# Optimization experiments

Hardware: AMD Instinct MI355X
Metric: run time of the kernel (lower is better)

## Reference

```python
import jax, jax.numpy as jnp
import numpy as np

T, F, H = 2048, 256, 384  # seq_len, input_size, hidden_size


def setup_inputs() -> dict:
    key = jax.random.key(0)
    ks = jax.random.split(key, 16)
    s = 1.0 / np.sqrt(F)
    d = {"x": jax.random.normal(ks[0], (T, F), jnp.float32)}
    names = ["q", "k", "v", "i", "f", "o"]
    for j, n in enumerate(names):
        d[f"W{n}"] = jax.random.uniform(ks[1 + j], (H, F), jnp.float32, -s, s)
        d[f"b{n}"] = jax.random.uniform(ks[7 + j], (H,), jnp.float32, -s, s)
    d["conv_w"] = jax.random.uniform(ks[13], (1, 1, 4), jnp.float32, -0.5, 0.5)
    d["conv_b"] = jax.random.uniform(ks[14], (1,), jnp.float32, -0.5, 0.5)
    return d


def _forward(x, Wq, bq, Wk, bk, Wv, bv, Wi, bi, Wf, bf, Wo, bo, conv_w, conv_b):
    # Conv1d(1->1, kernel=4, padding=(3,3)) along time, per input feature.
    xt = x.T[:, None, :]  # (F, 1, T)  feature axis acts as batch
    y = jax.lax.conv_general_dilated(xt, conv_w, (1,), [(3, 3)])  # (F, 1, T+3)
    xp = (y[:, 0, :] + conv_b[0]).T  # (T+3, F)

    inv_sqrt_h = 1.0 / jnp.sqrt(jnp.asarray(H, xp.dtype))
    # Precompute all per-step projections with dense GEMMs (time-parallel part).
    q = xp @ Wq.T + bq                      # (T+3, H)
    k = (xp @ Wk.T + bk) * inv_sqrt_h       # (T+3, H); extra bias_k is zero-init
    v = xp @ Wv.T + bv
    i = jnp.exp(xp @ Wi.T + bi)
    f = jax.nn.sigmoid(xp @ Wf.T + bf)
    o = jax.nn.sigmoid(xp @ Wo.T + bo)

    def step(carry, inp):
        C, n = carry                         # C: (H,H), n: (H,)
        qt, kt, vt, it, ft, ot = inp
        C = ft * C + it * jnp.outer(vt, kt)  # broadcast over last axis, as original
        n = ft * n + it * kt
        den = jnp.maximum(jnp.abs(jnp.dot(n, qt)), 1.0)
        h = ot * (C @ qt) / den
        return (C, n), h

    init = (jnp.zeros((H, H), xp.dtype), jnp.zeros((H,), xp.dtype))
    _, hs = jax.lax.scan(step, init, (q, k, v, i, f, o))
    return hs[-1]  # return_all=False -> last hidden state, shape (H,)


def reference(x, Wq, bq, Wk, bk, Wv, bv, Wi, bi, Wf, bf, Wo, bo, conv_w, conv_b):
    return _forward(x, Wq, bq, Wk, bk, Wv, bv, Wi, bi, Wf, bf, Wo, bo, conv_w, conv_b)
```

## Files before the change

kernel.cpp:

```cpp
#include <hip/hip_runtime.h>
#include <math.h>

#define T_IN 2048
#define TP   2051
#define F    256
#define H    384
#define BK   16
#define NT2  129
#define NCS  258
#define NC3  257

__device__ __forceinline__ float logsig(float z) {
    return (z >= 0.0f) ? -log1pf(__expf(-z)) : z - log1pf(__expf(z));
}

__global__ __launch_bounds__(256) void k1_conv(const float* __restrict__ x,
                        const float* __restrict__ cw,
                        const float* __restrict__ cb, float* __restrict__ xp) {
    int t = blockIdx.x * 4 + (threadIdx.x >> 6);
    int f4 = threadIdx.x & 63;
    if (t >= TP) return;
    float w[4] = {cw[0], cw[1], cw[2], cw[3]};
    float b = cb[0];
    float4 acc = {b, b, b, b};
    int i0 = t - 3;
    const float4* x4 = (const float4*)x;
    #pragma unroll
    for (int j = 0; j < 4; ++j) {
        int tt = i0 + j;
        if (tt >= 0 && tt < T_IN) {
            float4 xv = x4[tt * 64 + f4];
            acc.x = fmaf(w[j], xv.x, acc.x);
            acc.y = fmaf(w[j], xv.y, acc.y);
            acc.z = fmaf(w[j], xv.z, acc.z);
            acc.w = fmaf(w[j], xv.w, acc.w);
        }
    }
    ((float4*)xp)[t * 64 + f4] = acc;
}

__global__ __launch_bounds__(64) void k2_proj(
    const float* __restrict__ xp,
    const float* __restrict__ Wk, const float* __restrict__ bk,
    const float* __restrict__ Wi, const float* __restrict__ bi,
    const float* __restrict__ Wf, const float* __restrict__ bf,
    float* __restrict__ zk, float* __restrict__ ai, float* __restrict__ lf,
    float* __restrict__ cs) {
    __shared__ float alds[BK][20];
    __shared__ float wlds[3][BK][68];
    __shared__ float csred[4][68];
    int tid = threadIdx.x;
    int t0 = blockIdx.x * 16, b0 = blockIdx.y * 64;
    int tx = tid & 15, ty = tid >> 4;
    const float* Wg[3] = {Wk, Wi, Wf};
    float acc[3][16];
    #pragma unroll
    for (int j = 0; j < 3; ++j)
        #pragma unroll
        for (int u = 0; u < 16; ++u) acc[j][u] = 0.0f;

    int at = tid >> 2;
    int ak = (tid & 3) * 4;

    for (int k0 = 0; k0 < 256; k0 += BK) {
        __syncthreads();
        float4 xv = {0.f, 0.f, 0.f, 0.f};
        if (t0 + at < TP) xv = *(const float4*)&xp[(t0 + at) * 256 + k0 + ak];
        alds[ak + 0][at] = xv.x; alds[ak + 1][at] = xv.y;
        alds[ak + 2][at] = xv.z; alds[ak + 3][at] = xv.w;
        #pragma unroll
        for (int j = 0; j < 3; ++j) {
            #pragma unroll
            for (int h = 0; h < 4; ++h) {
                int row = h * 16 + at;
                float4 wv = *(const float4*)&Wg[j][(b0 + row) * 256 + k0 + ak];
                wlds[j][ak + 0][row] = wv.x; wlds[j][ak + 1][row] = wv.y;
                wlds[j][ak + 2][row] = wv.z; wlds[j][ak + 3][row] = wv.w;
            }
        }
        __syncthreads();
        #pragma unroll
        for (int kk = 0; kk < BK; ++kk) {
            float4 a4 = *(const float4*)&alds[kk][ty * 4];
            #pragma unroll
            for (int j = 0; j < 3; ++j) {
                float4 b4 = *(const float4*)&wlds[j][kk][tx * 4];
                acc[j][0]  = fmaf(a4.x, b4.x, acc[j][0]);
                acc[j][1]  = fmaf(a4.x, b4.y, acc[j][1]);
                acc[j][2]  = fmaf(a4.x, b4.z, acc[j][2]);
                acc[j][3]  = fmaf(a4.x, b4.w, acc[j][3]);
                acc[j][4]  = fmaf(a4.y, b4.x, acc[j][4]);
                acc[j][5]  = fmaf(a4.y, b4.y, acc[j][5]);
                acc[j][6]  = fmaf(a4.y, b4.z, acc[j][6]);
                acc[j][7]  = fmaf(a4.y, b4.w, acc[j][7]);
                acc[j][8]  = fmaf(a4.z, b4.x, acc[j][8]);
                acc[j][9]  = fmaf(a4.z, b4.y, acc[j][9]);
                acc[j][10] = fmaf(a4.z, b4.z, acc[j][10]);
                acc[j][11] = fmaf(a4.z, b4.w, acc[j][11]);
                acc[j][12] = fmaf(a4.w, b4.x, acc[j][12]);
                acc[j][13] = fmaf(a4.w, b4.y, acc[j][13]);
                acc[j][14] = fmaf(a4.w, b4.z, acc[j][14]);
                acc[j][15] = fmaf(a4.w, b4.w, acc[j][15]);
            }
        }
    }
    int bA = b0 + tx * 4;
    float4 bk4 = *(const float4*)&bk[bA];
    float4 bi4 = *(const float4*)&bi[bA];
    float4 bf4 = *(const float4*)&bf[bA];
    const float sc = 0.05103103630798287f;
    float4 lfs = {0.f, 0.f, 0.f, 0.f};
    #pragma unroll
    for (int tt = 0; tt < 4; ++tt) {
        int t = t0 + ty * 4 + tt;
        if (t < TP) {
            int row = t * H + bA;
            int o = tt * 4;
            float4 v;
            v.x = (acc[0][o+0] + bk4.x) * sc; v.y = (acc[0][o+1] + bk4.y) * sc;
            v.z = (acc[0][o+2] + bk4.z) * sc; v.w = (acc[0][o+3] + bk4.w) * sc;
            *(float4*)&zk[row] = v;
            v.x = acc[1][o+0] + bi4.x; v.y = acc[1][o+1] + bi4.y;
            v.z = acc[1][o+2] + bi4.z; v.w = acc[1][o+3] + bi4.w;
            *(float4*)&ai[row] = v;
            float4 l;
            l.x = logsig(acc[2][o+0] + bf4.x); l.y = logsig(acc[2][o+1] + bf4.y);
            l.z = logsig(acc[2][o+2] + bf4.z); l.w = logsig(acc[2][o+3] + bf4.w);
            *(float4*)&lf[row] = l;
            lfs.x += l.x; lfs.y += l.y; lfs.z += l.z; lfs.w += l.w;
        }
    }
    *(float4*)&csred[ty][tx * 4] = lfs;
    __syncthreads();
    {
        float s0 = csred[0][tid] + csred[1][tid];
        float s1 = csred[2][tid] + csred[3][tid];
        cs[(2 * blockIdx.x + 0) * H + b0 + tid] = s0;
        cs[(2 * blockIdx.x + 1) * H + b0 + tid] = s1;
    }
}

__global__ __launch_bounds__(256) void k2b_qo(const float* __restrict__ xp,
        const float* __restrict__ Wq, const float* __restrict__ bq,
        const float* __restrict__ Wo, const float* __restrict__ bo,
        float* __restrict__ q, float* __restrict__ o) {
    int tid = threadIdx.x;
    int lane = tid & 63;
    int row = blockIdx.x * 4 + (tid >> 6);
    float4 xv = *(const float4*)&xp[(TP - 1) * 256 + lane * 4];
    float4 q4 = *(const float4*)&Wq[row * 256 + lane * 4];
    float4 o4 = *(const float4*)&Wo[row * 256 + lane * 4];
    float aq = fmaf(xv.x, q4.x, fmaf(xv.y, q4.y, fmaf(xv.z, q4.z, xv.w * q4.w)));
    float ao = fmaf(xv.x, o4.x, fmaf(xv.y, o4.y, fmaf(xv.z, o4.z, xv.w * o4.w)));
    #pragma unroll
    for (int off = 32; off; off >>= 1) {
        aq += __shfl_down(aq, off, 64);
        ao += __shfl_down(ao, off, 64);
    }
    if (lane == 0) {
        q[row] = aq + bq[row];
        o[row] = 1.0f / (1.0f + __expf(-(ao + bo[row])));
    }
}

__global__ __launch_bounds__(64) void k3b_scan(const float* __restrict__ cs,
                                               float* __restrict__ co) {
    int b = blockIdx.x * 64 + threadIdx.x;
    float L = 0.0f;
    #pragma unroll 16
    for (int c = NCS - 1; c >= 0; --c) {
        co[c * H + b] = L;
        L += cs[c * H + b];
    }
}

__global__ __launch_bounds__(384) void k3_fused(
    const float* __restrict__ ai, const float* __restrict__ lf,
    const float* __restrict__ zk, const float* __restrict__ co,
    const float* __restrict__ q, const float* __restrict__ xp,
    float* __restrict__ zf, float* __restrict__ Gf) {
    __shared__ float zred[6][256];
    __shared__ float gred[6];
    int tid = threadIdx.x;
    int w = tid >> 6, lane = tid & 63;
    int c = blockIdx.x, ts = c * 8;
    float co0 = co[c * H + tid];
    float qb = q[tid];
    float aiv[8], lfv[8], zkv[8];
    float4 xv[8];
    if (ts + 8 <= TP) {
        #pragma unroll
        for (int u = 0; u < 8; ++u) {
            int idx = (ts + u) * H + tid;
            aiv[u] = ai[idx]; lfv[u] = lf[idx]; zkv[u] = zk[idx];
            xv[u] = *(const float4*)&xp[(ts + u) * 256 + lane * 4];
        }
    } else {
        #pragma unroll
        for (int u = 0; u < 8; ++u) {
            if (ts + u < TP) {
                int idx = (ts + u) * H + tid;
                aiv[u] = ai[idx]; lfv[u] = lf[idx]; zkv[u] = zk[idx];
                xv[u] = *(const float4*)&xp[(ts + u) * 256 + lane * 4];
            } else {
                aiv[u] = -1e30f; lfv[u] = 0.f; zkv[u] = 0.f;
                xv[u].x = xv[u].y = xv[u].z = xv[u].w = 0.f;
            }
        }
    }
    float S = 0.f, gsum = 0.f;
    float z0 = 0.f, z1 = 0.f, z2 = 0.f, z3 = 0.f;
    #pragma unroll
    for (int u = 7; u >= 0; --u) {
        float wv = __expf(aiv[u] + co0 + S) * zkv[u] * qb;
        S += lfv[u];
        float s = wv;
        s += __shfl_xor(s, 1, 64);
        s += __shfl_xor(s, 2, 64);
        s += __shfl_xor(s, 4, 64);
        s += __shfl_xor(s, 8, 64);
        s += __shfl_xor(s, 16, 64);
        s += __shfl_xor(s, 32, 64);
        gsum += s;
        z0 = fmaf(s, xv[u].x, z0);
        z1 = fmaf(s, xv[u].y, z1);
        z2 = fmaf(s, xv[u].z, z2);
        z3 = fmaf(s, xv[u].w, z3);
    }
    zred[w][lane * 4 + 0] = z0;
    zred[w][lane * 4 + 1] = z1;
    zred[w][lane * 4 + 2] = z2;
    zred[w][lane * 4 + 3] = z3;
    if (lane == 0) gred[w] = gsum;
    __syncthreads();
    if (tid < 256) {
        float s = zred[0][tid] + zred[1][tid] + zred[2][tid]
                + zred[3][tid] + zred[4][tid] + zred[5][tid];
        atomicAdd(&zf[tid], s);
    }
    if (tid == 0)
        atomicAdd(Gf, gred[0] + gred[1] + gred[2] + gred[3] + gred[4] + gred[5]);
}

__global__ __launch_bounds__(256) void k6_out(const float* __restrict__ zf,
        const float* __restrict__ Gf,
        const float* __restrict__ Wv, const float* __restrict__ bv,
        const float* __restrict__ o, float* __restrict__ out) {
    int tid = threadIdx.x;
    int lane = tid & 63;
    int row = blockIdx.x * 4 + (tid >> 6);
    float Gv = Gf[0];
    float4 zv = *(const float4*)&zf[lane * 4];
    float4 wv = *(const float4*)&Wv[row * 256 + lane * 4];
    float acc = fmaf(zv.x, wv.x, fmaf(zv.y, wv.y, fmaf(zv.z, wv.z, zv.w * wv.w)));
    #pragma unroll
    for (int off = 32; off; off >>= 1) acc += __shfl_down(acc, off, 64);
    if (lane == 0)
        out[row] = o[row] * (acc + bv[row] * Gv) / fmaxf(fabsf(Gv), 1.0f);
}

extern "C" void kernel_launch(void* const* d_in, const int* in_sizes, int n_in,
                              void* d_out, int out_size, void* d_ws, size_t ws_size,
                              hipStream_t stream) {
    const float* x  = (const float*)d_in[0];
    const float* Wq = (const float*)d_in[1];  const float* bq = (const float*)d_in[2];
    const float* Wk = (const float*)d_in[3];  const float* bk = (const float*)d_in[4];
    const float* Wv = (const float*)d_in[5];  const float* bv = (const float*)d_in[6];
    const float* Wi = (const float*)d_in[7];  const float* bi = (const float*)d_in[8];
    const float* Wf = (const float*)d_in[9];  const float* bf = (const float*)d_in[10];
    const float* Wo = (const float*)d_in[11]; const float* bo = (const float*)d_in[12];
    const float* cw = (const float*)d_in[13]; const float* cb = (const float*)d_in[14];
    float* out = (float*)d_out;

    float* ws = (float*)d_ws;
    float* xp  = ws;
    float* zk  = xp  + TP * F;
    float* ai  = zk  + TP * H;
    float* lf  = ai  + TP * H;
    float* cs  = lf  + TP * H;
    float* co  = cs  + NCS * H;
    float* qv  = co  + NCS * H;
    float* ov  = qv  + H;
    float* zf  = ov  + H;
    float* Gf  = zf  + F;

    hipMemsetAsync((void*)zf, 0, (F + 4) * sizeof(float), stream);
    k1_conv<<<(TP + 3) / 4, 256, 0, stream>>>(x, cw, cb, xp);
    k2_proj<<<dim3(NT2, 6), 64, 0, stream>>>(xp, Wk, bk, Wi, bi, Wf, bf, zk, ai, lf, cs);
    k2b_qo<<<96, 256, 0, stream>>>(xp, Wq, bq, Wo, bo, qv, ov);
    k3b_scan<<<6, 64, 0, stream>>>(cs, co);
    k3_fused<<<NC3, 384, 0, stream>>>(ai, lf, zk, co, qv, xp, zf, Gf);
    k6_out<<<96, 256, 0, stream>>>(zf, Gf, Wv, bv, ov, out);
}
```

Before: 174.1 us.

## Retile projection GEMM to smaller time tiles with double-buffered LDS prefetch

```diff
diff --git a/kernel.cpp b/kernel.cpp
--- a/kernel.cpp
+++ b/kernel.cpp
@@ -6,8 +6,8 @@
 #define F    256
 #define H    384
 #define BK   16
-#define NT2  129
-#define NCS  258
+#define NT2  257
+#define NCS  257
 #define NC3  257
 
 __device__ __forceinline__ float logsig(float z) {
@@ -39,104 +39,97 @@
     ((float4*)xp)[t * 64 + f4] = acc;
 }
 
-__global__ __launch_bounds__(64) void k2_proj(
+__global__ __launch_bounds__(256) void k2_proj(
     const float* __restrict__ xp,
     const float* __restrict__ Wk, const float* __restrict__ bk,
     const float* __restrict__ Wi, const float* __restrict__ bi,
     const float* __restrict__ Wf, const float* __restrict__ bf,
     float* __restrict__ zk, float* __restrict__ ai, float* __restrict__ lf,
     float* __restrict__ cs) {
-    __shared__ float alds[BK][20];
-    __shared__ float wlds[3][BK][68];
-    __shared__ float csred[4][68];
-    int tid = threadIdx.x;
-    int t0 = blockIdx.x * 16, b0 = blockIdx.y * 64;
-    int tx = tid & 15, ty = tid >> 4;
-    const float* Wg[3] = {Wk, Wi, Wf};
-    float acc[3][16];
-    #pragma unroll
-    for (int j = 0; j < 3; ++j)
-        #pragma unroll
-        for (int u = 0; u < 16; ++u) acc[j][u] = 0.0f;
-
-    int at = tid >> 2;
-    int ak = (tid & 3) * 4;
-
-    for (int k0 = 0; k0 < 256; k0 += BK) {
+    __shared__ float alds[2][BK][12];
+    __shared__ float wlds[2][3][BK][66];
+    __shared__ float csred[8][66];
+    int tid = threadIdx.x;
+    int t0 = blockIdx.x * 8, b0 = blockIdx.y * 64;
+    int tx = tid & 31, ty = tid >> 5;
+    float2 acc0 = {0.f, 0.f}, acc1 = {0.f, 0.f}, acc2 = {0.f, 0.f};
+
+    int wrow = tid >> 2;
+    int wk4 = (tid & 3) * 4;
+    int grow = (b0 + wrow) * 256 + wk4;
+    int arow = (t0 + (tid >> 2)) * 256 + wk4;
+    bool aval = (tid < 32) && (t0 + (tid >> 2) < TP);
+
+    float4 aw = {0.f, 0.f, 0.f, 0.f}, ww0, ww1, ww2;
+    if (aval) aw = *(const float4*)&xp[arow];
+    ww0 = *(const float4*)&Wk[grow];
+    ww1 = *(const float4*)&Wi[grow];
+    ww2 = *(const float4*)&Wf[grow];
+
+    for (int i = 0; i < 16; ++i) {
+        int buf = i & 1;
+        if (tid < 32) {
+            int tq = tid >> 2;
+            alds[buf][wk4 + 0][tq] = aw.x;
+            alds[buf][wk4 + 1][tq] = aw.y;
+            alds[buf][wk4 + 2][tq] = aw.z;
+            alds[buf][wk4 + 3][tq] = aw.w;
+        }
+        wlds[buf][0][wk4 + 0][wrow] = ww0.x;
+        wlds[buf][0][wk4 + 1][wrow] = ww0.y;
+        wlds[buf][0][wk4 + 2][wrow] = ww0.z;
+        wlds[buf][0][wk4 + 3][wrow] = ww0.w;
+        wlds[buf][1][wk4 + 0][wrow] = ww1.x;
+        wlds[buf][1][wk4 + 1][wrow] = ww1.y;
+        wlds[buf][1][wk4 + 2][wrow] = ww1.z;
+        wlds[buf][1][wk4 + 3][wrow] = ww1.w;
+        wlds[buf][2][wk4 + 0][wrow] = ww2.x;
+        wlds[buf][2][wk4 + 1][wrow] = ww2.y;
+        wlds[buf][2][wk4 + 2][wrow] = ww2.z;
+        wlds[buf][2][wk4 + 3][wrow] = ww2.w;
         __syncthreads();
-        float4 xv = {0.f, 0.f, 0.f, 0.f};
-        if (t0 + at < TP) xv = *(const float4*)&xp[(t0 + at) * 256 + k0 + ak];
-        alds[ak + 0][at] = xv.x; alds[ak + 1][at] = xv.y;
-        alds[ak + 2][at] = xv.z; alds[ak + 3][at] = xv.w;
-        #pragma unroll
-        for (int j = 0; j < 3; ++j) {
-            #pragma unroll
-            for (int h = 0; h < 4; ++h) {
-                int row = h * 16 + at;
-                float4 wv = *(const float4*)&Wg[j][(b0 + row) * 256 + k0 + ak];
-                wlds[j][ak + 0][row] = wv.x; wlds[j][ak + 1][row] = wv.y;
-                wlds[j][ak + 2][row] = wv.z; wlds[j][ak + 3][row] = wv.w;
-            }
-        }
-        __syncthreads();
+        if (i < 15) {
+            int k0 = (i + 1) * BK;
+            if (aval) aw = *(const float4*)&xp[arow + k0];
+            ww0 = *(const float4*)&Wk[grow + k0];
+            ww1 = *(const float4*)&Wi[grow + k0];
+            ww2 = *(const float4*)&Wf[grow + k0];
+        }
         #pragma unroll
         for (int kk = 0; kk < BK; ++kk) {
-            float4 a4 = *(const float4*)&alds[kk][ty * 4];
-            #pragma unroll
-            for (int j = 0; j < 3; ++j) {
-                float4 b4 = *(const float4*)&wlds[j][kk][tx * 4];
-                acc[j][0]  = fmaf(a4.x, b4.x, acc[j][0]);
-                acc[j][1]  = fmaf(a4.x, b4.y, acc[j][1]);
-                acc[j][2]  = fmaf(a4.x, b4.z, acc[j][2]);
-                acc[j][3]  = fmaf(a4.x, b4.w, acc[j][3]);
-                acc[j][4]  = fmaf(a4.y, b4.x, acc[j][4]);
-                acc[j][5]  = fmaf(a4.y, b4.y, acc[j][5]);
-                acc[j][6]  = fmaf(a4.y, b4.z, acc[j][6]);
-                acc[j][7]  = fmaf(a4.y, b4.w, acc[j][7]);
-                acc[j][8]  = fmaf(a4.z, b4.x, acc[j][8]);
-                acc[j][9]  = fmaf(a4.z, b4.y, acc[j][9]);
-                acc[j][10] = fmaf(a4.z, b4.z, acc[j][10]);
-                acc[j][11] = fmaf(a4.z, b4.w, acc[j][11]);
-                acc[j][12] = fmaf(a4.w, b4.x, acc[j][12]);
-                acc[j][13] = fmaf(a4.w, b4.y, acc[j][13]);
-                acc[j][14] = fmaf(a4.w, b4.z, acc[j][14]);
-                acc[j][15] = fmaf(a4.w, b4.w, acc[j][15]);
-            }
-        }
-    }
-    int bA = b0 + tx * 4;
-    float4 bk4 = *(const float4*)&bk[bA];
-    float4 bi4 = *(const float4*)&bi[bA];
-    float4 bf4 = *(const float4*)&bf[bA];
-    const float sc = 0.05103103630798287f;
-    float4 lfs = {0.f, 0.f, 0.f, 0.f};
-    #pragma unroll
-    for (int tt = 0; tt < 4; ++tt) {
-        int t = t0 + ty * 4 + tt;
-        if (t < TP) {
-            int row = t * H + bA;
-            int o = tt * 4;
-            float4 v;
-            v.x = (acc[0][o+0] + bk4.x) * sc; v.y = (acc[0][o+1] + bk4.y) * sc;
-            v.z = (acc[0][o+2] + bk4.z) * sc; v.w = (acc[0][o+3] + bk4.w) * sc;
-            *(float4*)&zk[row] = v;
-            v.x = acc[1][o+0] + bi4.x; v.y = acc[1][o+1] + bi4.y;
-            v.z = acc[1][o+2] + bi4.z; v.w = acc[1][o+3] + bi4.w;
-            *(float4*)&ai[row] = v;
-            float4 l;
-            l.x = logsig(acc[2][o+0] + bf4.x); l.y = logsig(acc[2][o+1] + bf4.y);
-            l.z = logsig(acc[2][o+2] + bf4.z); l.w = logsig(acc[2][o+3] + bf4.w);
-            *(float4*)&lf[row] = l;
-            lfs.x += l.x; lfs.y += l.y; lfs.z += l.z; lfs.w += l.w;
-        }
-    }
-    *(float4*)&csred[ty][tx * 4] = lfs;
+            float a = alds[buf][kk][ty];
+            float2 b0v = *(const float2*)&wlds[buf][0][kk][2 * tx];
+            float2 b1v = *(const float2*)&wlds[buf][1][kk][2 * tx];
+            float2 b2v = *(const float2*)&wlds[buf][2][kk][2 * tx];
+            acc0.x = fmaf(a, b0v.x, acc0.x); acc0.y = fmaf(a, b0v.y, acc0.y);
+            acc1.x = fmaf(a, b1v.x, acc1.x); acc1.y = fmaf(a, b1v.y, acc1.y);
+            acc2.x = fmaf(a, b2v.x, acc2.x); acc2.y = fmaf(a, b2v.y, acc2.y);
+        }
+    }
+    int bA = b0 + 2 * tx;
+    int t = t0 + ty;
+    float2 l2 = {0.f, 0.f};
+    if (t < TP) {
+        float2 bk2 = *(const float2*)&bk[bA];
+        float2 bi2 = *(const float2*)&bi[bA];
+        float2 bf2 = *(const float2*)&bf[bA];
+        const float sc = 0.05103103630798287f;
+        int row = t * H + bA;
+        float2 v;
+        v.x = (acc0.x + bk2.x) * sc; v.y = (acc0.y + bk2.y) * sc;
+        *(float2*)&zk[row] = v;
+        v.x = acc1.x + bi2.x; v.y = acc1.y + bi2.y;
+        *(float2*)&ai[row] = v;
+        l2.x = logsig(acc2.x + bf2.x); l2.y = logsig(acc2.y + bf2.y);
+        *(float2*)&lf[row] = l2;
+    }
+    *(float2*)&csred[ty][2 * tx] = l2;
     __syncthreads();
-    {
-        float s0 = csred[0][tid] + csred[1][tid];
-        float s1 = csred[2][tid] + csred[3][tid];
-        cs[(2 * blockIdx.x + 0) * H + b0 + tid] = s0;
-        cs[(2 * blockIdx.x + 1) * H + b0 + tid] = s1;
+    if (tid < 64) {
+        float s = 0.f;
+        #pragma unroll
+        for (int y = 0; y < 8; ++y) s += csred[y][tid];
+        cs[blockIdx.x * H + b0 + tid] = s;
     }
 }
 
@@ -286,8 +279,8 @@
 
     hipMemsetAsync((void*)zf, 0, (F + 4) * sizeof(float), stream);
     k1_conv<<<(TP + 3) / 4, 256, 0, stream>>>(x, cw, cb, xp);
-    k2_proj<<<dim3(NT2, 6), 64, 0, stream>>>(xp, Wk, bk, Wi, bi, Wf, bf, zk, ai, lf, cs);
     k2b_qo<<<96, 256, 0, stream>>>(xp, Wq, bq, Wo, bo, qv, ov);
+    k2_proj<<<dim3(NT2, 6), 256, 0, stream>>>(xp, Wk, bk, Wi, bi, Wf, bf, zk, ai, lf, cs);
     k3b_scan<<<6, 64, 0, stream>>>(cs, co);
     k3_fused<<<NC3, 384, 0, stream>>>(ai, lf, zk, co, qv, xp, zf, Gf);
     k6_out<<<96, 256, 0, stream>>>(zf, Gf, Wv, bv, ov, out);
```

Measured after the change: 174.1 us. Within noise of the previous version (-0.0%).

## Merge conv, q/o projection and zeroing into one prep kernel; pre-transpose gate weights

Applied to the files above, without the earlier changes.

```diff
diff --git a/kernel.cpp b/kernel.cpp
--- a/kernel.cpp
+++ b/kernel.cpp
@@ -5,161 +5,170 @@
 #define TP   2051
 #define F    256
 #define H    384
-#define BK   16
 #define NT2  129
 #define NCS  258
 #define NC3  257
+#define WTS  (256 * 384)
 
 __device__ __forceinline__ float logsig(float z) {
     return (z >= 0.0f) ? -log1pf(__expf(-z)) : z - log1pf(__expf(z));
 }
 
-__global__ __launch_bounds__(256) void k1_conv(const float* __restrict__ x,
-                        const float* __restrict__ cw,
-                        const float* __restrict__ cb, float* __restrict__ xp) {
-    int t = blockIdx.x * 4 + (threadIdx.x >> 6);
-    int f4 = threadIdx.x & 63;
-    if (t >= TP) return;
-    float w[4] = {cw[0], cw[1], cw[2], cw[3]};
-    float b = cb[0];
-    float4 acc = {b, b, b, b};
-    int i0 = t - 3;
-    const float4* x4 = (const float4*)x;
-    #pragma unroll
-    for (int j = 0; j < 4; ++j) {
-        int tt = i0 + j;
-        if (tt >= 0 && tt < T_IN) {
-            float4 xv = x4[tt * 64 + f4];
-            acc.x = fmaf(w[j], xv.x, acc.x);
-            acc.y = fmaf(w[j], xv.y, acc.y);
-            acc.z = fmaf(w[j], xv.z, acc.z);
-            acc.w = fmaf(w[j], xv.w, acc.w);
-        }
-    }
-    ((float4*)xp)[t * 64 + f4] = acc;
-}
-
-__global__ __launch_bounds__(64) void k2_proj(
-    const float* __restrict__ xp,
-    const float* __restrict__ Wk, const float* __restrict__ bk,
-    const float* __restrict__ Wi, const float* __restrict__ bi,
-    const float* __restrict__ Wf, const float* __restrict__ bf,
+__global__ __launch_bounds__(256) void prep(
+    const float* __restrict__ x, const float* __restrict__ cw, const float* __restrict__ cb,
+    const float* __restrict__ Wk, const float* __restrict__ Wi, const float* __restrict__ Wf,
+    const float* __restrict__ Wq, const float* __restrict__ bq,
+    const float* __restrict__ Wo, const float* __restrict__ bo,
+    float* __restrict__ xp, float* __restrict__ Wt,
+    float* __restrict__ qv, float* __restrict__ ov, float* __restrict__ zf) {
+    int bx = blockIdx.x, tid = threadIdx.x;
+    if (bx < 513) {
+        int t = bx * 4 + (tid >> 6);
+        int f4 = tid & 63;
+        if (t >= TP) return;
+        float w0 = cw[0], w1 = cw[1], w2 = cw[2], w3 = cw[3];
+        float b = cb[0];
+        float4 acc = {b, b, b, b};
+        int i0 = t - 3;
+        const float4* x4 = (const float4*)x;
+        float wj[4] = {w0, w1, w2, w3};
+        #pragma unroll
+        for (int j = 0; j < 4; ++j) {
+            int tt = i0 + j;
+            if (tt >= 0 && tt < T_IN) {
+                float4 xv = x4[tt * 64 + f4];
+                acc.x = fmaf(wj[j], xv.x, acc.x);
+                acc.y = fmaf(wj[j], xv.y, acc.y);
+                acc.z = fmaf(wj[j], xv.z, acc.z);
+                acc.w = fmaf(wj[j], xv.w, acc.w);
+            }
+        }
+        ((float4*)xp)[t * 64 + f4] = acc;
+    } else if (bx < 801) {
+        __shared__ float tl[32][33];
+        int tb = bx - 513;
+        int j = tb / 96, rem = tb % 96;
+        int k0 = (rem / 12) * 32, b0 = (rem % 12) * 32;
+        const float* W = (j == 0) ? Wk : (j == 1) ? Wi : Wf;
+        int c = tid & 31, r0 = tid >> 5;
+        #pragma unroll
+        for (int s = 0; s < 4; ++s) {
+            int r = r0 + 8 * s;
+            tl[r][c] = W[(b0 + r) * 256 + k0 + c];
+        }
+        __syncthreads();
+        float* dst = Wt + j * WTS;
+        #pragma unroll
+        for (int s = 0; s < 4; ++s) {
+            int rr = r0 + 8 * s;
+            dst[(k0 + rr) * 384 + b0 + c] = tl[c][rr];
+        }
+    } else if (bx < 897) {
+        int lane = tid & 63;
+        int row = (bx - 801) * 4 + (tid >> 6);
+        float b = cb[0];
+        float4 xv = {b, b, b, b};
+        #pragma unroll
+        for (int j = 0; j < 4; ++j) {
+            int tt = (TP - 1) - 3 + j;
+            if (tt >= 0 && tt < T_IN) {
+                float wj = cw[j];
+                float4 xr = *(const float4*)&x[tt * 256 + lane * 4];
+                xv.x = fmaf(wj, xr.x, xv.x);
+                xv.y = fmaf(wj, xr.y, xv.y);
+                xv.z = fmaf(wj, xr.z, xv.z);
+                xv.w = fmaf(wj, xr.w, xv.w);
+            }
+        }
+        float4 q4 = *(const float4*)&Wq[row * 256 + lane * 4];
+        float4 o4 = *(const float4*)&Wo[row * 256 + lane * 4];
+        float aq = fmaf(xv.x, q4.x, fmaf(xv.y, q4.y, fmaf(xv.z, q4.z, xv.w * q4.w)));
+        float ao = fmaf(xv.x, o4.x, fmaf(xv.y, o4.y, fmaf(xv.z, o4.z, xv.w * o4.w)));
+        #pragma unroll
+        for (int off = 32; off; off >>= 1) {
+            aq += __shfl_down(aq, off, 64);
+            ao += __shfl_down(ao, off, 64);
+        }
+        if (lane == 0) {
+            qv[row] = aq + bq[row];
+            ov[row] = 1.0f / (1.0f + __expf(-(ao + bo[row])));
+        }
+    } else {
+        zf[tid] = 0.0f;
+        if (tid == 0) zf[256] = 0.0f;
+    }
+}
+
+__global__ __launch_bounds__(256) void k2_proj(
+    const float* __restrict__ xp, const float* __restrict__ Wt,
+    const float* __restrict__ bk, const float* __restrict__ bi, const float* __restrict__ bf,
     float* __restrict__ zk, float* __restrict__ ai, float* __restrict__ lf,
     float* __restrict__ cs) {
-    __shared__ float alds[BK][20];
-    __shared__ float wlds[3][BK][68];
-    __shared__ float csred[4][68];
+    __shared__ float xl[16][260];
+    __shared__ float csred[16][68];
     int tid = threadIdx.x;
     int t0 = blockIdx.x * 16, b0 = blockIdx.y * 64;
     int tx = tid & 15, ty = tid >> 4;
-    const float* Wg[3] = {Wk, Wi, Wf};
-    float acc[3][16];
     #pragma unroll
-    for (int j = 0; j < 3; ++j)
-        #pragma unroll
-        for (int u = 0; u < 16; ++u) acc[j][u] = 0.0f;
-
-    int at = tid >> 2;
-    int ak = (tid & 3) * 4;
-
-    for (int k0 = 0; k0 < 256; k0 += BK) {
-        __syncthreads();
-        float4 xv = {0.f, 0.f, 0.f, 0.f};
-        if (t0 + at < TP) xv = *(const float4*)&xp[(t0 + at) * 256 + k0 + ak];
-        alds[ak + 0][at] = xv.x; alds[ak + 1][at] = xv.y;
-        alds[ak + 2][at] = xv.z; alds[ak + 3][at] = xv.w;
-        #pragma unroll
-        for (int j = 0; j < 3; ++j) {
-            #pragma unroll
-            for (int h = 0; h < 4; ++h) {
-                int row = h * 16 + at;
-                float4 wv = *(const float4*)&Wg[j][(b0 + row) * 256 + k0 + ak];
-                wlds[j][ak + 0][row] = wv.x; wlds[j][ak + 1][row] = wv.y;
-                wlds[j][ak + 2][row] = wv.z; wlds[j][ak + 3][row] = wv.w;
-            }
-        }
-        __syncthreads();
-        #pragma unroll
-        for (int kk = 0; kk < BK; ++kk) {
-            float4 a4 = *(const float4*)&alds[kk][ty * 4];
-            #pragma unroll
-            for (int j = 0; j < 3; ++j) {
-                float4 b4 = *(const float4*)&wlds[j][kk][tx * 4];
-                acc[j][0]  = fmaf(a4.x, b4.x, acc[j][0]);
-                acc[j][1]  = fmaf(a4.x, b4.y, acc[j][1]);
-                acc[j][2]  = fmaf(a4.x, b4.z, acc[j][2]);
-                acc[j][3]  = fmaf(a4.x, b4.w, acc[j][3]);
-                acc[j][4]  = fmaf(a4.y, b4.x, acc[j][4]);
-                acc[j][5]  = fmaf(a4.y, b4.y, acc[j][5]);
-                acc[j][6]  = fmaf(a4.y, b4.z, acc[j][6]);
-                acc[j][7]  = fmaf(a4.y, b4.w, acc[j][7]);
-                acc[j][8]  = fmaf(a4.z, b4.x, acc[j][8]);
-                acc[j][9]  = fmaf(a4.z, b4.y, acc[j][9]);
-                acc[j][10] = fmaf(a4.z, b4.z, acc[j][10]);
-                acc[j][11] = fmaf(a4.z, b4.w, acc[j][11]);
-                acc[j][12] = fmaf(a4.w, b4.x, acc[j][12]);
-                acc[j][13] = fmaf(a4.w, b4.y, acc[j][13]);
-                acc[j][14] = fmaf(a4.w, b4.z, acc[j][14]);
-                acc[j][15] = fmaf(a4.w, b4.w, acc[j][15]);
-            }
-        }
-    }
-    int bA = b0 + tx * 4;
-    float4 bk4 = *(const float4*)&bk[bA];
-    float4 bi4 = *(const float4*)&bi[bA];
-    float4 bf4 = *(const float4*)&bf[bA];
-    const float sc = 0.05103103630798287f;
-    float4 lfs = {0.f, 0.f, 0.f, 0.f};
-    #pragma unroll
-    for (int tt = 0; tt < 4; ++tt) {
-        int t = t0 + ty * 4 + tt;
-        if (t < TP) {
-            int row = t * H + bA;
-            int o = tt * 4;
-            float4 v;
-            v.x = (acc[0][o+0] + bk4.x) * sc; v.y = (acc[0][o+1] + bk4.y) * sc;
-            v.z = (acc[0][o+2] + bk4.z) * sc; v.w = (acc[0][o+3] + bk4.w) * sc;
-            *(float4*)&zk[row] = v;
-            v.x = acc[1][o+0] + bi4.x; v.y = acc[1][o+1] + bi4.y;
-            v.z = acc[1][o+2] + bi4.z; v.w = acc[1][o+3] + bi4.w;
-            *(float4*)&ai[row] = v;
-            float4 l;
-            l.x = logsig(acc[2][o+0] + bf4.x); l.y = logsig(acc[2][o+1] + bf4.y);
-            l.z = logsig(acc[2][o+2] + bf4.z); l.w = logsig(acc[2][o+3] + bf4.w);
-            *(float4*)&lf[row] = l;
-            lfs.x += l.x; lfs.y += l.y; lfs.z += l.z; lfs.w += l.w;
-        }
-    }
-    *(float4*)&csred[ty][tx * 4] = lfs;
+    for (int q = 0; q < 4; ++q) {
+        int flat = (tid + 256 * q) * 4;
+        int r = flat >> 8, k = flat & 255;
+        float4 v = {0.f, 0.f, 0.f, 0.f};
+        if (t0 + r < TP) v = *(const float4*)&xp[(t0 + r) * 256 + k];
+        *(float4*)&xl[r][k] = v;
+    }
     __syncthreads();
-    {
-        float s0 = csred[0][tid] + csred[1][tid];
-        float s1 = csred[2][tid] + csred[3][tid];
-        cs[(2 * blockIdx.x + 0) * H + b0 + tid] = s0;
-        cs[(2 * blockIdx.x + 1) * H + b0 + tid] = s1;
-    }
-}
-
-__global__ __launch_bounds__(256) void k2b_qo(const float* __restrict__ xp,
-        const float* __restrict__ Wq, const float* __restrict__ bq,
-        const float* __restrict__ Wo, const float* __restrict__ bo,
-        float* __restrict__ q, float* __restrict__ o) {
-    int tid = threadIdx.x;
-    int lane = tid & 63;
-    int row = blockIdx.x * 4 + (tid >> 6);
-    float4 xv = *(const float4*)&xp[(TP - 1) * 256 + lane * 4];
-    float4 q4 = *(const float4*)&Wq[row * 256 + lane * 4];
-    float4 o4 = *(const float4*)&Wo[row * 256 + lane * 4];
-    float aq = fmaf(xv.x, q4.x, fmaf(xv.y, q4.y, fmaf(xv.z, q4.z, xv.w * q4.w)));
-    float ao = fmaf(xv.x, o4.x, fmaf(xv.y, o4.y, fmaf(xv.z, o4.z, xv.w * o4.w)));
-    #pragma unroll
-    for (int off = 32; off; off >>= 1) {
-        aq += __shfl_down(aq, off, 64);
-        ao += __shfl_down(ao, off, 64);
-    }
-    if (lane == 0) {
-        q[row] = aq + bq[row];
-        o[row] = 1.0f / (1.0f + __expf(-(ao + bo[row])));
+    int c0 = b0 + 4 * tx;
+    const float* pk = Wt + 0 * WTS + c0;
+    const float* pi = Wt + 1 * WTS + c0;
+    const float* pf = Wt + 2 * WTS + c0;
+    float4 a0 = {0.f, 0.f, 0.f, 0.f}, a1 = a0, a2 = a0;
+    #pragma unroll 2
+    for (int k4 = 0; k4 < 256; k4 += 4) {
+        float4 av = *(const float4*)&xl[ty][k4];
+        float acar[4] = {av.x, av.y, av.z, av.w};
+        #pragma unroll
+        for (int u = 0; u < 4; ++u) {
+            int kk = k4 + u;
+            float a = acar[u];
+            float4 bkv = *(const float4*)&pk[kk * 384];
+            float4 biv = *(const float4*)&pi[kk * 384];
+            float4 bfv = *(const float4*)&pf[kk * 384];
+            a0.x = fmaf(a, bkv.x, a0.x); a0.y = fmaf(a, bkv.y, a0.y);
+            a0.z = fmaf(a, bkv.z, a0.z); a0.w = fmaf(a, bkv.w, a0.w);
+            a1.x = fmaf(a, biv.x, a1.x); a1.y = fmaf(a, biv.y, a1.y);
+            a1.z = fmaf(a, biv.z, a1.z); a1.w = fmaf(a, biv.w, a1.w);
+            a2.x = fmaf(a, bfv.x, a2.x); a2.y = fmaf(a, bfv.y, a2.y);
+            a2.z = fmaf(a, bfv.z, a2.z); a2.w = fmaf(a, bfv.w, a2.w);
+        }
+    }
+    int t = t0 + ty;
+    float4 l4 = {0.f, 0.f, 0.f, 0.f};
+    if (t < TP) {
+        float4 bk4 = *(const float4*)&bk[c0];
+        float4 bi4 = *(const float4*)&bi[c0];
+        float4 bf4 = *(const float4*)&bf[c0];
+        const float sc = 0.05103103630798287f;
+        int row = t * H + c0;
+        float4 v;
+        v.x = (a0.x + bk4.x) * sc; v.y = (a0.y + bk4.y) * sc;
+        v.z = (a0.z + bk4.z) * sc; v.w = (a0.w + bk4.w) * sc;
+        *(float4*)&zk[row] = v;
+        v.x = a1.x + bi4.x; v.y = a1.y + bi4.y;
+        v.z = a1.z + bi4.z; v.w = a1.w + bi4.w;
+        *(float4*)&ai[row] = v;
+        l4.x = logsig(a2.x + bf4.x); l4.y = logsig(a2.y + bf4.y);
+        l4.z = logsig(a2.z + bf4.z); l4.w = logsig(a2.w + bf4.w);
+        *(float4*)&lf[row] = l4;
+    }
+    *(float4*)&csred[ty][4 * tx] = l4;
+    __syncthreads();
+    if (tid < 128) {
+        int half = tid >> 6, col = tid & 63;
+        float s = 0.f;
+        #pragma unroll
+        for (int r = 0; r < 8; ++r) s += csred[half * 8 + r][col];
+        cs[(2 * blockIdx.x + half) * H + b0 + col] = s;
     }
 }
 
@@ -274,7 +283,8 @@
 
     float* ws = (float*)d_ws;
     float* xp  = ws;
-    float* zk  = xp  + TP * F;
+    float* Wt  = xp  + TP * F;
+    float* zk  = Wt  + 3 * WTS;
     float* ai  = zk  + TP * H;
     float* lf  = ai  + TP * H;
     float* cs  = lf  + TP * H;
@@ -284,10 +294,9 @@
     float* zf  = ov  + H;
     float* Gf  = zf  + F;
 
-    hipMemsetAsync((void*)zf, 0, (F + 4) * sizeof(float), stream);
-    k1_conv<<<(TP + 3) / 4, 256, 0, stream>>>(x, cw, cb, xp);
-    k2_proj<<<dim3(NT2, 6), 64, 0, stream>>>(xp, Wk, bk, Wi, bi, Wf, bf, zk, ai, lf, cs);
-    k2b_qo<<<96, 256, 0, stream>>>(xp, Wq, bq, Wo, bo, qv, ov);
+    prep<<<898, 256, 0, stream>>>(x, cw, cb, Wk, Wi, Wf, Wq, bq, Wo, bo,
+                                  xp, Wt, qv, ov, zf);
+    k2_proj<<<dim3(NT2, 6), 256, 0, stream>>>(xp, Wt, bk, bi, bf, zk, ai, lf, cs);
     k3b_scan<<<6, 64, 0, stream>>>(cs, co);
     k3_fused<<<NC3, 384, 0, stream>>>(ai, lf, zk, co, qv, xp, zf, Gf);
     k6_out<<<96, 256, 0, stream>>>(zf, Gf, Wv, bv, ov, out);
```

After: 205.8 us. 1.18x slower.
